# Optimization experiments

Measured on AMD Instinct MI355X. Metric: run time of the kernel, lower is better.

The kernel has to match this reference:

```python
import jax, jax.numpy as jnp
import numpy as np

XYZ_MIN = np.array([-1.0, -1.0, -1.0], np.float32)
XYZ_MAX = np.array([1.0, 1.0, 1.0], np.float32)
N_SAMPLES = 256
T_NEAR, T_FAR = 0.05, 2.0
ALPHA_INIT = 1e-6
ACT_SHIFT = float(np.log(1.0 / (1.0 - ALPHA_INIT) - 1.0))  # density bias shift
INTERVAL = 0.5  # stepsize * voxel_size_ratio
VIEWBASE_PE = 4


def trilerp(grid, pts):
    """grid: [C, X, Y, Z]; pts: [P, 3] world coords. Returns [P, C]."""
    res = jnp.asarray(grid.shape[1:], dtype=pts.dtype)  # [3]
    ind = (pts - XYZ_MIN) / (XYZ_MAX - XYZ_MIN) * (res - 1.0)
    ind = jnp.clip(ind, 0.0, res - 1.0)
    i0 = jnp.minimum(jnp.floor(ind), res - 2.0).astype(jnp.int32)  # [P,3]
    f = ind - i0.astype(pts.dtype)  # [P,3] fractional offsets
    x0, y0, z0 = i0[:, 0], i0[:, 1], i0[:, 2]
    x1, y1, z1 = x0 + 1, y0 + 1, z0 + 1
    fx, fy, fz = f[:, 0], f[:, 1], f[:, 2]
    gx, gy, gz = 1.0 - fx, 1.0 - fy, 1.0 - fz
    out = (grid[:, x0, y0, z0] * (gx * gy * gz)
           + grid[:, x1, y0, z0] * (fx * gy * gz)
           + grid[:, x0, y1, z0] * (gx * fy * gz)
           + grid[:, x0, y0, z1] * (gx * gy * fz)
           + grid[:, x1, y1, z0] * (fx * fy * gz)
           + grid[:, x1, y0, z1] * (fx * gy * fz)
           + grid[:, x0, y1, z1] * (gx * fy * fz)
           + grid[:, x1, y1, z1] * (fx * fy * fz))  # [C,P]
    return out.T


def setup_inputs() -> dict:
    key = jax.random.key(0)
    ks = jax.random.split(key, 10)
    N = 4096
    rays_o = jax.random.normal(ks[0], (N, 3), jnp.float32) * 0.05
    rays_d = jax.random.normal(ks[1], (N, 3), jnp.float32)
    density = jax.random.normal(ks[2], (1, 1, 160, 160, 160), jnp.float32)
    k0 = jax.random.normal(ks[3], (1, 12, 160, 160, 160), jnp.float32) * 0.1
    w0 = jax.random.normal(ks[4], (39, 128), jnp.float32) * (1.0 / np.sqrt(39))
    b0 = jnp.zeros((128,), jnp.float32)
    w1 = jax.random.normal(ks[5], (128, 128), jnp.float32) * (1.0 / np.sqrt(128))
    b1 = jnp.zeros((128,), jnp.float32)
    w2 = jax.random.normal(ks[6], (128, 3), jnp.float32) * (1.0 / np.sqrt(128))
    b2 = jnp.zeros((3,), jnp.float32)
    return {"rays_o": rays_o, "rays_d": rays_d, "density": density, "k0": k0,
            "w0": w0, "b0": b0, "w1": w1, "b1": b1, "w2": w2, "b2": b2}


def reference(rays_o, rays_d, density, k0, w0, b0, w1, b1, w2, b2):
    N = rays_o.shape[0]
    dens_grid = density[0]            # [1,X,Y,Z]
    feat_grid = k0[0]                 # [C,X,Y,Z]
    viewdirs = rays_d / jnp.linalg.norm(rays_d, axis=-1, keepdims=True)
    t = jnp.linspace(T_NEAR, T_FAR, N_SAMPLES, dtype=rays_o.dtype)  # [S]
    pts = rays_o[:, None, :] + viewdirs[:, None, :] * t[None, :, None]  # [N,S,3]
    inbox = jnp.all((pts >= XYZ_MIN) & (pts <= XYZ_MAX), axis=-1)  # [N,S]
    flat = pts.reshape(-1, 3)

    # density -> alpha: 1 - (1 + exp(d + shift))^(-interval)   (Raw2Alpha)
    d = trilerp(dens_grid, flat)[:, 0].reshape(N, N_SAMPLES)
    alpha = 1.0 - jnp.power(1.0 + jnp.exp(d + ACT_SHIFT), -INTERVAL)
    alpha = jnp.where(inbox, alpha, 0.0)

    # alpha -> weights via exclusive transmittance cumprod (Alphas2Weights)
    T_full = jnp.cumprod(1.0 - alpha, axis=1)               # [N,S]
    T_excl = jnp.concatenate([jnp.ones((N, 1), alpha.dtype), T_full[:, :-1]], axis=1)
    weights = alpha * T_excl                                 # [N,S]
    alphainv_last = T_full[:, -1]                            # [N]

    # color features + view-direction positional encoding
    feat = trilerp(feat_grid, flat).reshape(N, N_SAMPLES, -1)  # [N,S,C]
    freqs = (2.0 ** jnp.arange(VIEWBASE_PE)).astype(rays_o.dtype)
    vf = viewdirs[:, :, None] * freqs[None, None, :]           # [N,3,PE]
    vemb = jnp.concatenate([viewdirs, jnp.sin(vf).reshape(N, -1), jnp.cos(vf).reshape(N, -1)], axis=-1)  # [N,27]
    x = jnp.concatenate([feat, jnp.broadcast_to(vemb[:, None, :], (N, N_SAMPLES, vemb.shape[-1]))], axis=-1)

    h = jax.nn.relu(x @ w0 + b0)
    h = jax.nn.relu(h @ w1 + b1)
    rgb = jax.nn.sigmoid(h @ w2 + b2)                          # [N,S,3]

    rgb_marched = jnp.einsum('ns,nsc->nc', weights, rgb) + alphainv_last[:, None] * 1.0  # white bg
    return rgb_marched
```

## Files before the change

kernel.cpp:

```cpp
#include <hip/hip_runtime.h>
#include <hip/hip_bf16.h>
#include <math.h>

#define ACT_SHIFT_F (-13.8155095579637744f)
#define GRID_VOX 4096000
#define GP_BYTES  (GRID_VOX * 32)
#define W0P_OFF   GP_BYTES
#define W1P_OFF   (W0P_OFF + 8 * 1024)
#define W2P_OFF   (W1P_OFF + 32 * 1024)
#define WS_NEED   ((size_t)(W2P_OFF + 4 * 1024))

typedef __bf16 bf16x8 __attribute__((ext_vector_type(8)));
typedef float  f32x4  __attribute__((ext_vector_type(4)));

__device__ __forceinline__ float bfu(unsigned short b) {
    return __uint_as_float(((unsigned int)b) << 16);
}
__device__ __forceinline__ unsigned short f2bf(float x) {
    unsigned int u = __float_as_uint(x);
    u += 0x7fffu + ((u >> 16) & 1u);
    return (unsigned short)(u >> 16);
}
#define UNPK(u, lo, hi) { lo = __uint_as_float((u) << 16); hi = __uint_as_float((u) & 0xffff0000u); }

__device__ __constant__ int offv_c[8] = {0, 1, 160, 161, 25600, 25601, 25760, 25761};

__global__ void repack_all(const float* __restrict__ dens, const float* __restrict__ k0,
                           const float* __restrict__ w0, const float* __restrict__ w1,
                           const float* __restrict__ w2,
                           unsigned short* __restrict__ gp, unsigned short* __restrict__ wp)
{
    const int b = blockIdx.x;
    if (b < 16000) {
        const int v = b * 256 + threadIdx.x;
        unsigned short s[16];
        s[0] = f2bf(dens[v]);
        #pragma unroll
        for (int c = 0; c < 12; ++c) s[1 + c] = f2bf(k0[c * GRID_VOX + v]);
        s[13] = 0; s[14] = 0; s[15] = 0;
        uint4 q0, q1;
        q0.x = s[0] | (s[1] << 16);  q0.y = s[2] | (s[3] << 16);
        q0.z = s[4] | (s[5] << 16);  q0.w = s[6] | (s[7] << 16);
        q1.x = s[8] | (s[9] << 16);  q1.y = s[10] | (s[11] << 16);
        q1.z = s[12] | (s[13] << 16); q1.w = s[14] | (s[15] << 16);
        uint4* dst = (uint4*)(gp + (size_t)v * 16);
        dst[0] = q0; dst[1] = q1;
        return;
    }
    const int t = (b - 16000) * 256 + threadIdx.x;
    if (t >= 44 * 64) return;
    const int f = t >> 6, l = t & 63;
    const int n16 = l & 15, kg = l >> 4;
    unsigned short v[8];
    if (f < 8) {
        const int n = f * 16 + n16;
        #pragma unroll
        for (int j = 0; j < 8; ++j) {
            const int k = kg * 8 + j;
            v[j] = (k < 12) ? f2bf(w0[k * 128 + n]) : (unsigned short)0;
        }
    } else if (f < 40) {
        const int ff = f - 8, nt = ff >> 2, ks = ff & 3;
        const int n = nt * 16 + n16;
        #pragma unroll
        for (int j = 0; j < 8; ++j) {
            const int k = ks * 32 + kg * 8 + j;
            v[j] = f2bf(w1[k * 128 + n]);
        }
    } else {
        const int ks = f - 40;
        #pragma unroll
        for (int j = 0; j < 8; ++j) {
            const int k = ks * 32 + kg * 8 + j;
            v[j] = (n16 < 3) ? f2bf(w2[k * 3 + n16]) : (unsigned short)0;
        }
    }
    uint4 q;
    q.x = v[0] | (v[1] << 16); q.y = v[2] | (v[3] << 16);
    q.z = v[4] | (v[5] << 16); q.w = v[6] | (v[7] << 16);
    *(uint4*)(wp + f * 512 + l * 8) = q;
}

__global__ __launch_bounds__(256, 3)
void dvgo_mfma(const float* __restrict__ rays_o, const float* __restrict__ rays_d,
               const float* __restrict__ w0, const float* __restrict__ b0,
               const float* __restrict__ b1, const float* __restrict__ b2,
               const unsigned short* __restrict__ gp,
               const unsigned short* __restrict__ wpk,
               float* __restrict__ out)
{
    __shared__ unsigned short Xs[128 * 40];
    __shared__ unsigned short Hs[128 * 136];
    __shared__ float sh[256];
    __shared__ float wts[256];
    __shared__ float b0eff[128];
    __shared__ float b1s[128];
    __shared__ float vemb[28];
    __shared__ float red[4][3];
    __shared__ float b2s[3];
    __shared__ float ainv_sh;

    const int r = blockIdx.x, t = threadIdx.x;
    const int l = t & 63, wv = t >> 6;
    const int col = l & 15, rg = l >> 4;

    const float ox = rays_o[r*3+0], oy = rays_o[r*3+1], oz = rays_o[r*3+2];
    const float dxr = rays_d[r*3+0], dyr = rays_d[r*3+1], dzr = rays_d[r*3+2];
    const float rn = rsqrtf(dxr*dxr + dyr*dyr + dzr*dzr);
    const float vx = dxr*rn, vy = dyr*rn, vz = dzr*rn;

    if (t < 27) {
        float val;
        if (t < 3) val = (t == 0) ? vx : ((t == 1) ? vy : vz);
        else {
            int q = t - 3;
            const bool is_sin = q < 12;
            if (!is_sin) q -= 12;
            const int i = q >> 2, p = q & 3;
            const float a = ((i == 0) ? vx : ((i == 1) ? vy : vz)) * (float)(1 << p);
            val = is_sin ? sinf(a) : cosf(a);
        }
        vemb[t] = val;
    }
    if (t < 3)   b2s[t] = b2[t];
    if (t < 128) b1s[t] = b1[t];

    float alpha = 0.f;
    {
        const float tp = 0.05f + (1.95f / 255.f) * (float)t;
        const float px = ox + vx*tp, py = oy + vy*tp, pz = oz + vz*tp;
        const bool inbox = (px >= -1.f) & (px <= 1.f) & (py >= -1.f) & (py <= 1.f) &
                           (pz >= -1.f) & (pz <= 1.f);
        if (inbox) {
            const float ix = fminf(fmaxf((px + 1.f) * 79.5f, 0.f), 159.f);
            const float iy = fminf(fmaxf((py + 1.f) * 79.5f, 0.f), 159.f);
            const float iz = fminf(fmaxf((pz + 1.f) * 79.5f, 0.f), 159.f);
            const int x0 = min((int)ix, 158), y0 = min((int)iy, 158), z0 = min((int)iz, 158);
            const float fx = ix - x0, fy = iy - y0, fz = iz - z0;
            const float gx = 1.f - fx, gy = 1.f - fy, gz = 1.f - fz;
            const int base = (x0 * 160 + y0) * 160 + z0;
            float w8[8];
            w8[0]=gx*gy*gz; w8[1]=gx*gy*fz; w8[2]=gx*fy*gz; w8[3]=gx*fy*fz;
            w8[4]=fx*gy*gz; w8[5]=fx*gy*fz; w8[6]=fx*fy*gz; w8[7]=fx*fy*fz;
            float d = 0.f;
            #pragma unroll
            for (int cn = 0; cn < 8; ++cn)
                d = fmaf(w8[cn], bfu(gp[(size_t)(base + offv_c[cn]) * 16]), d);
            const float e = expf(d + ACT_SHIFT_F);
            const float op = 1.f + e;
            alpha = e / (op + sqrtf(op));
        }
        sh[t] = 1.f - alpha;
    }
    __syncthreads();

    if (t < 128) {
        float a = b0[t];
        #pragma unroll
        for (int k = 0; k < 27; ++k) a = fmaf(vemb[k], w0[(12 + k) * 128 + t], a);
        b0eff[t] = a;
    }
    for (int i = t; i < 128 * 10; i += 256) {
        const int row = i / 10, c = i % 10;
        ((unsigned int*)Xs)[row * 20 + 6 + c] = 0u;
    }

    #pragma unroll
    for (int off = 1; off < 256; off <<= 1) {
        const float v = (t >= off) ? sh[t - off] : 1.f;
        __syncthreads();
        sh[t] *= v;
        __syncthreads();
    }
    wts[t] = alpha * ((t == 0) ? 1.f : sh[t - 1]);
    if (t == 255) ainv_sh = sh[255];

    const unsigned short* w0p = wpk;
    const unsigned short* w1p = wpk + 8 * 512;
    const unsigned short* w2p = wpk + 40 * 512;
    const uint4* gq = (const uint4*)gp;

    float pacc = 0.f;

    #pragma unroll 1
    for (int ck = 0; ck < 2; ++ck) {
        {
            const int sl = t >> 1, hf = t & 1;
            const int s = ck * 128 + sl;
            const float tp = 0.05f + (1.95f / 255.f) * (float)s;
            const float px = ox + vx*tp, py = oy + vy*tp, pz = oz + vz*tp;
            const bool inbox = (px >= -1.f) & (px <= 1.f) & (py >= -1.f) & (py <= 1.f) &
                               (pz >= -1.f) & (pz <= 1.f);
            unsigned short* xrow = &Xs[sl * 40];
            if (inbox) {
                const float ix = fminf(fmaxf((px + 1.f) * 79.5f, 0.f), 159.f);
                const float iy = fminf(fmaxf((py + 1.f) * 79.5f, 0.f), 159.f);
                const float iz = fminf(fmaxf((pz + 1.f) * 79.5f, 0.f), 159.f);
                const int x0 = min((int)ix, 158), y0 = min((int)iy, 158), z0 = min((int)iz, 158);
                const float fx = ix - x0, fy = iy - y0, fz = iz - z0;
                const float gx = 1.f - fx, gy = 1.f - fy, gz = 1.f - fz;
                const int base = (x0 * 160 + y0) * 160 + z0;
                float w8[8];
                w8[0]=gx*gy*gz; w8[1]=gx*gy*fz; w8[2]=gx*fy*gz; w8[3]=gx*fy*fz;
                w8[4]=fx*gy*gz; w8[5]=fx*gy*fz; w8[6]=fx*fy*gz; w8[7]=fx*fy*fz;
                float a0=0,a1=0,a2=0,a3=0,a4=0,a5=0,a6=0,a7=0;
                #pragma unroll
                for (int cn = 0; cn < 8; ++cn) {
                    const uint4 q = gq[(size_t)(base + offv_c[cn]) * 2 + hf];
                    float f0,f1,f2,f3,f4,f5,f6,f7;
                    UNPK(q.x, f0, f1); UNPK(q.y, f2, f3);
                    UNPK(q.z, f4, f5); UNPK(q.w, f6, f7);
                    const float wc = w8[cn];
                    a0=fmaf(wc,f0,a0); a1=fmaf(wc,f1,a1); a2=fmaf(wc,f2,a2); a3=fmaf(wc,f3,a3);
                    a4=fmaf(wc,f4,a4); a5=fmaf(wc,f5,a5); a6=fmaf(wc,f6,a6); a7=fmaf(wc,f7,a7);
                }
                if (hf == 0) {
                    xrow[0]=f2bf(a1); xrow[1]=f2bf(a2); xrow[2]=f2bf(a3); xrow[3]=f2bf(a4);
                    xrow[4]=f2bf(a5); xrow[5]=f2bf(a6); xrow[6]=f2bf(a7);
                } else {
                    xrow[7]=f2bf(a0); xrow[8]=f2bf(a1); xrow[9]=f2bf(a2);
                    xrow[10]=f2bf(a3); xrow[11]=f2bf(a4);
                }
            } else {
                if (hf == 0) {
                    #pragma unroll
                    for (int j = 0; j < 7; ++j) xrow[j] = 0;
                } else {
                    #pragma unroll
                    for (int j = 7; j < 12; ++j) xrow[j] = 0;
                }
            }
        }
        __syncthreads();

        const int row0 = wv * 32;

        {
            bf16x8 A0[2];
            #pragma unroll
            for (int mt = 0; mt < 2; ++mt)
                A0[mt] = *(const bf16x8*)(&Xs[(row0 + mt * 16 + col) * 40 + rg * 8]);
            #pragma unroll 1
            for (int nt = 0; nt < 8; ++nt) {
                const bf16x8 B = *(const bf16x8*)(w0p + nt * 512 + l * 8);
                const float bias = b0eff[nt * 16 + col];
                #pragma unroll
                for (int mt = 0; mt < 2; ++mt) {
                    f32x4 acc = {0.f, 0.f, 0.f, 0.f};
                    acc = __builtin_amdgcn_mfma_f32_16x16x32_bf16(A0[mt], B, acc, 0, 0, 0);
                    #pragma unroll
                    for (int q = 0; q < 4; ++q) {
                        const float v  = fmaxf(acc[q] + bias, 0.f);
                        const float vo = __shfl_xor(v, 1);
                        if ((l & 1) == 0) {
                            const int row = row0 + mt * 16 + rg * 4 + q;
                            const unsigned int pk = (unsigned int)f2bf(v) |
                                                    ((unsigned int)f2bf(vo) << 16);
                            *(unsigned int*)(&Hs[row * 136 + nt * 16 + col]) = pk;
                        }
                    }
                }
            }
        }

        {
            bf16x8 A1[2][4];
            #pragma unroll
            for (int mt = 0; mt < 2; ++mt)
                #pragma unroll
                for (int ks = 0; ks < 4; ++ks)
                    A1[mt][ks] = *(const bf16x8*)(&Hs[(row0 + mt * 16 + col) * 136 + ks * 32 + rg * 8]);
            #pragma unroll 1
            for (int nt = 0; nt < 8; ++nt) {
                bf16x8 Bk[4];
                #pragma unroll
                for (int ks = 0; ks < 4; ++ks)
                    Bk[ks] = *(const bf16x8*)(w1p + (nt * 4 + ks) * 512 + l * 8);
                const float bias = b1s[nt * 16 + col];
                #pragma unroll
                for (int mt = 0; mt < 2; ++mt) {
                    f32x4 acc = {0.f, 0.f, 0.f, 0.f};
                    #pragma unroll
                    for (int ks = 0; ks < 4; ++ks)
                        acc = __builtin_amdgcn_mfma_f32_16x16x32_bf16(A1[mt][ks], Bk[ks], acc, 0, 0, 0);
                    #pragma unroll
                    for (int q = 0; q < 4; ++q) {
                        const float v  = fmaxf(acc[q] + bias, 0.f);
                        const float vo = __shfl_xor(v, 1);
                        if ((l & 1) == 0) {
                            const int row = row0 + mt * 16 + rg * 4 + q;
                            const unsigned int pk = (unsigned int)f2bf(v) |
                                                    ((unsigned int)f2bf(vo) << 16);
                            *(unsigned int*)(&Hs[row * 136 + nt * 16 + col]) = pk;
                        }
                    }
                }
            }
        }

        {
            bf16x8 Bk[4];
            #pragma unroll
            for (int ks = 0; ks < 4; ++ks)
                Bk[ks] = *(const bf16x8*)(w2p + ks * 512 + l * 8);
            const float bias2 = (col < 3) ? b2s[col] : 0.f;
            #pragma unroll
            for (int mt = 0; mt < 2; ++mt) {
                bf16x8 A2[4];
                #pragma unroll
                for (int ks = 0; ks < 4; ++ks)
                    A2[ks] = *(const bf16x8*)(&Hs[(row0 + mt * 16 + col) * 136 + ks * 32 + rg * 8]);
                f32x4 acc = {0.f, 0.f, 0.f, 0.f};
                #pragma unroll
                for (int ks = 0; ks < 4; ++ks)
                    acc = __builtin_amdgcn_mfma_f32_16x16x32_bf16(A2[ks], Bk[ks], acc, 0, 0, 0);
                #pragma unroll
                for (int q = 0; q < 4; ++q) {
                    const float rv = acc[q] + bias2;
                    const float sg = 1.f / (1.f + expf(-rv));
                    const int srow = ck * 128 + row0 + mt * 16 + rg * 4 + q;
                    pacc = fmaf(wts[srow], sg, pacc);
                }
            }
        }
        __syncthreads();
    }

    pacc += __shfl_xor(pacc, 16);
    pacc += __shfl_xor(pacc, 32);
    if (rg == 0 && col < 3) red[wv][col] = pacc;
    __syncthreads();
    if (t < 3) out[r * 3 + t] = red[0][t] + red[1][t] + red[2][t] + red[3][t] + ainv_sh;
}

__global__ __launch_bounds__(256, 2)
void dvgo_render(const float* __restrict__ rays_o, const float* __restrict__ rays_d,
                 const float* __restrict__ dens, const float* __restrict__ k0,
                 const float* __restrict__ w0, const float* __restrict__ b0,
                 const float* __restrict__ w1, const float* __restrict__ b1,
                 const float* __restrict__ w2, const float* __restrict__ b2,
                 float* __restrict__ out)
{
    __shared__ float xs[256 * 40];
    __shared__ float sh[256];
    __shared__ float wts[256];
    __shared__ float h0s[2][128];
    __shared__ float red[2][2][3];
    __shared__ float rgbacc[6];
    __shared__ float ainv_sh;

    const int r = blockIdx.x, tid = threadIdx.x;
    {
        const int s = tid;
        const float ox = rays_o[r*3+0], oy = rays_o[r*3+1], oz = rays_o[r*3+2];
        const float dxr = rays_d[r*3+0], dyr = rays_d[r*3+1], dzr = rays_d[r*3+2];
        const float rn = rsqrtf(dxr*dxr + dyr*dyr + dzr*dzr);
        const float vx = dxr*rn, vy = dyr*rn, vz = dzr*rn;
        const float t = 0.05f + 1.95f * (1.0f/255.0f) * (float)s;
        const float px = ox + vx*t, py = oy + vy*t, pz = oz + vz*t;
        const bool inbox = (px >= -1.f) && (px <= 1.f) && (py >= -1.f) && (py <= 1.f) &&
                           (pz >= -1.f) && (pz <= 1.f);
        const float ix = fminf(fmaxf((px + 1.f) * 79.5f, 0.f), 159.f);
        const float iy = fminf(fmaxf((py + 1.f) * 79.5f, 0.f), 159.f);
        const float iz = fminf(fmaxf((pz + 1.f) * 79.5f, 0.f), 159.f);
        const int x0 = min((int)ix, 158), y0 = min((int)iy, 158), z0 = min((int)iz, 158);
        const float fx = ix - x0, fy = iy - y0, fz = iz - z0;
        const float gx = 1.f - fx, gy = 1.f - fy, gz = 1.f - fz;
        const int DX = 25600, DY = 160;
        const int base = (x0*160 + y0)*160 + z0;
        const float w000=gx*gy*gz, w100=fx*gy*gz, w010=gx*fy*gz, w001=gx*gy*fz;
        const float w110=fx*fy*gz, w101=fx*gy*fz, w011=gx*fy*fz, w111=fx*fy*fz;
        float alpha = 0.f;
        if (inbox) {
            const float d = dens[base]*w000 + dens[base+DX]*w100 + dens[base+DY]*w010 +
                            dens[base+1]*w001 + dens[base+DX+DY]*w110 + dens[base+DX+1]*w101 +
                            dens[base+DY+1]*w011 + dens[base+DX+DY+1]*w111;
            const float e = expf(d + ACT_SHIFT_F);
            const float op = 1.f + e;
            alpha = e / (op + sqrtf(op));
        }
        sh[s] = 1.f - alpha;
        __syncthreads();
        #pragma unroll
        for (int off = 1; off < 256; off <<= 1) {
            const float v = (s >= off) ? sh[s - off] : 1.f;
            __syncthreads();
            sh[s] *= v;
            __syncthreads();
        }
        wts[s] = alpha * ((s == 0) ? 1.f : sh[s-1]);
        if (s == 255) ainv_sh = sh[255];
        if (s < 6) rgbacc[s] = 0.f;
        float* xrow = &xs[s*40];
        if (inbox) {
            #pragma unroll
            for (int c = 0; c < 12; ++c) {
                const float* g = k0 + c*4096000 + base;
                xrow[c] = g[0]*w000 + g[DX]*w100 + g[DY]*w010 + g[1]*w001 +
                          g[DX+DY]*w110 + g[DX+1]*w101 + g[DY+1]*w011 + g[DX+DY+1]*w111;
            }
        } else {
            #pragma unroll
            for (int c = 0; c < 12; ++c) xrow[c] = 0.f;
        }
        xrow[12]=vx; xrow[13]=vy; xrow[14]=vz;
        const float v3[3] = {vx, vy, vz};
        #pragma unroll
        for (int i = 0; i < 3; ++i)
            #pragma unroll
            for (int p = 0; p < 4; ++p) {
                const float a = v3[i] * (float)(1 << p);
                xrow[15 + i*4 + p] = sinf(a);
                xrow[27 + i*4 + p] = cosf(a);
            }
        xrow[39] = 0.f;
    }
    __syncthreads();
    const int j = tid & 127, sb = tid >> 7;
    float w0c[40];
    #pragma unroll
    for (int k = 0; k < 39; ++k) w0c[k] = w0[k*128 + j];
    w0c[39] = 0.f;
    float w1c[128];
    #pragma unroll
    for (int k = 0; k < 128; ++k) w1c[k] = w1[k*128 + j];
    const float b0j = b0[j], b1j = b1[j];
    const float w2r0 = w2[j*3+0], w2r1 = w2[j*3+1], w2r2 = w2[j*3+2];
    const float b20 = b2[0], b21 = b2[1], b22 = b2[2];
    const int lane = tid & 63, halfw = (tid >> 6) & 1;
    for (int it = 0; it < 128; ++it) {
        const int s = it*2 + sb;
        const float4* xrow4 = (const float4*)(&xs[s*40]);
        float acc = b0j;
        #pragma unroll
        for (int q = 0; q < 10; ++q) {
            const float4 v = xrow4[q];
            acc = fmaf(v.x, w0c[q*4+0], acc); acc = fmaf(v.y, w0c[q*4+1], acc);
            acc = fmaf(v.z, w0c[q*4+2], acc); acc = fmaf(v.w, w0c[q*4+3], acc);
        }
        h0s[sb][j] = fmaxf(acc, 0.f);
        __syncthreads();
        float acc1 = b1j;
        const float4* h4 = (const float4*)(&h0s[sb][0]);
        #pragma unroll
        for (int q = 0; q < 32; ++q) {
            const float4 v = h4[q];
            acc1 = fmaf(v.x, w1c[q*4+0], acc1); acc1 = fmaf(v.y, w1c[q*4+1], acc1);
            acc1 = fmaf(v.z, w1c[q*4+2], acc1); acc1 = fmaf(v.w, w1c[q*4+3], acc1);
        }
        const float hv = fmaxf(acc1, 0.f);
        float p0 = hv*w2r0, p1 = hv*w2r1, p2 = hv*w2r2;
        #pragma unroll
        for (int off = 32; off > 0; off >>= 1) {
            p0 += __shfl_down(p0, off); p1 += __shfl_down(p1, off); p2 += __shfl_down(p2, off);
        }
        if (lane == 0) { red[sb][halfw][0]=p0; red[sb][halfw][1]=p1; red[sb][halfw][2]=p2; }
        __syncthreads();
        if (tid == sb*128) {
            const float r0 = red[sb][0][0]+red[sb][1][0]+b20;
            const float r1 = red[sb][0][1]+red[sb][1][1]+b21;
            const float r2 = red[sb][0][2]+red[sb][1][2]+b22;
            const float wgt = wts[s];
            rgbacc[sb*3+0] += wgt / (1.f + expf(-r0));
            rgbacc[sb*3+1] += wgt / (1.f + expf(-r1));
            rgbacc[sb*3+2] += wgt / (1.f + expf(-r2));
        }
    }
    __syncthreads();
    if (tid < 3) out[r*3 + tid] = rgbacc[tid] + rgbacc[3 + tid] + ainv_sh;
}

extern "C" void kernel_launch(void* const* d_in, const int* in_sizes, int n_in,
                              void* d_out, int out_size, void* d_ws, size_t ws_size,
                              hipStream_t stream)
{
    const float* rays_o = (const float*)d_in[0];
    const float* rays_d = (const float*)d_in[1];
    const float* dens   = (const float*)d_in[2];
    const float* k0     = (const float*)d_in[3];
    const float* w0     = (const float*)d_in[4];
    const float* b0     = (const float*)d_in[5];
    const float* w1     = (const float*)d_in[6];
    const float* b1     = (const float*)d_in[7];
    const float* w2     = (const float*)d_in[8];
    const float* b2     = (const float*)d_in[9];
    float* out = (float*)d_out;
    const int N = in_sizes[0] / 3;

    if (ws_size >= WS_NEED) {
        unsigned short* gp  = (unsigned short*)d_ws;
        unsigned short* wpk = (unsigned short*)((char*)d_ws + W0P_OFF);
        repack_all<<<dim3(16011), dim3(256), 0, stream>>>(dens, k0, w0, w1, w2, gp, wpk);
        dvgo_mfma<<<dim3(N), dim3(256), 0, stream>>>(rays_o, rays_d, w0, b0, b1, b2,
                                                     gp, wpk, out);
    } else {
        dvgo_render<<<dim3(N), dim3(256), 0, stream>>>(rays_o, rays_d, dens, k0,
                                                       w0, b0, w1, b1, w2, b2, out);
    }
}
```

Measured before the change: 515.2 us.

## Vectorize grid repack and fuse alpha computation into per-chunk feature gather

```diff
diff --git a/kernel.cpp b/kernel.cpp
--- a/kernel.cpp
+++ b/kernel.cpp
@@ -12,6 +12,7 @@
 
 typedef __bf16 bf16x8 __attribute__((ext_vector_type(8)));
 typedef float  f32x4  __attribute__((ext_vector_type(4)));
+typedef float  fv4    __attribute__((ext_vector_type(4)));
 
 __device__ __forceinline__ float bfu(unsigned short b) {
     return __uint_as_float(((unsigned int)b) << 16);
@@ -20,6 +21,9 @@
     unsigned int u = __float_as_uint(x);
     u += 0x7fffu + ((u >> 16) & 1u);
     return (unsigned short)(u >> 16);
+}
+__device__ __forceinline__ unsigned int packtr(float a, float b) {
+    return (__float_as_uint(a) >> 16) | (__float_as_uint(b) & 0xffff0000u);
 }
 #define UNPK(u, lo, hi) { lo = __uint_as_float((u) << 16); hi = __uint_as_float((u) & 0xffff0000u); }
 
@@ -31,23 +35,32 @@
                            unsigned short* __restrict__ gp, unsigned short* __restrict__ wp)
 {
     const int b = blockIdx.x;
-    if (b < 16000) {
-        const int v = b * 256 + threadIdx.x;
-        unsigned short s[16];
-        s[0] = f2bf(dens[v]);
-        #pragma unroll
-        for (int c = 0; c < 12; ++c) s[1 + c] = f2bf(k0[c * GRID_VOX + v]);
-        s[13] = 0; s[14] = 0; s[15] = 0;
-        uint4 q0, q1;
-        q0.x = s[0] | (s[1] << 16);  q0.y = s[2] | (s[3] << 16);
-        q0.z = s[4] | (s[5] << 16);  q0.w = s[6] | (s[7] << 16);
-        q1.x = s[8] | (s[9] << 16);  q1.y = s[10] | (s[11] << 16);
-        q1.z = s[12] | (s[13] << 16); q1.w = s[14] | (s[15] << 16);
-        uint4* dst = (uint4*)(gp + (size_t)v * 16);
-        dst[0] = q0; dst[1] = q1;
+    if (b < 4000) {
+        const int v4 = b * 1024 + threadIdx.x * 4;
+        const fv4 d4 = __builtin_nontemporal_load((const fv4*)(dens + v4));
+        fv4 c4[12];
+        #pragma unroll
+        for (int c = 0; c < 12; ++c)
+            c4[c] = __builtin_nontemporal_load((const fv4*)(k0 + (size_t)c * GRID_VOX + v4));
+        uint4* dst = (uint4*)(gp + (size_t)v4 * 16);
+        #pragma unroll
+        for (int j = 0; j < 4; ++j) {
+            const float* cj = &((const float*)c4)[j];
+            uint4 q0, q1;
+            q0.x = packtr(d4[j],    cj[0]);
+            q0.y = packtr(cj[4*1],  cj[4*2]);
+            q0.z = packtr(cj[4*3],  cj[4*4]);
+            q0.w = packtr(cj[4*5],  cj[4*6]);
+            q1.x = packtr(cj[4*7],  cj[4*8]);
+            q1.y = packtr(cj[4*9],  cj[4*10]);
+            q1.z = packtr(cj[4*11], 0.f);
+            q1.w = 0u;
+            dst[j*2 + 0] = q0;
+            dst[j*2 + 1] = q1;
+        }
         return;
     }
-    const int t = (b - 16000) * 256 + threadIdx.x;
+    const int t = (b - 4000) * 256 + threadIdx.x;
     if (t >= 44 * 64) return;
     const int f = t >> 6, l = t & 63;
     const int n16 = l & 15, kg = l >> 4;
@@ -91,14 +104,15 @@
 {
     __shared__ unsigned short Xs[128 * 40];
     __shared__ unsigned short Hs[128 * 136];
-    __shared__ float sh[256];
-    __shared__ float wts[256];
+    __shared__ float shA[128];
+    __shared__ float wts[128];
     __shared__ float b0eff[128];
     __shared__ float b1s[128];
     __shared__ float vemb[28];
     __shared__ float red[4][3];
     __shared__ float b2s[3];
-    __shared__ float ainv_sh;
+    __shared__ float Tcs[3];
+    __shared__ float spart;
 
     const int r = blockIdx.x, t = threadIdx.x;
     const int l = t & 63, wv = t >> 6;
@@ -124,34 +138,7 @@
     }
     if (t < 3)   b2s[t] = b2[t];
     if (t < 128) b1s[t] = b1[t];
-
-    float alpha = 0.f;
-    {
-        const float tp = 0.05f + (1.95f / 255.f) * (float)t;
-        const float px = ox + vx*tp, py = oy + vy*tp, pz = oz + vz*tp;
-        const bool inbox = (px >= -1.f) & (px <= 1.f) & (py >= -1.f) & (py <= 1.f) &
-                           (pz >= -1.f) & (pz <= 1.f);
-        if (inbox) {
-            const float ix = fminf(fmaxf((px + 1.f) * 79.5f, 0.f), 159.f);
-            const float iy = fminf(fmaxf((py + 1.f) * 79.5f, 0.f), 159.f);
-            const float iz = fminf(fmaxf((pz + 1.f) * 79.5f, 0.f), 159.f);
-            const int x0 = min((int)ix, 158), y0 = min((int)iy, 158), z0 = min((int)iz, 158);
-            const float fx = ix - x0, fy = iy - y0, fz = iz - z0;
-            const float gx = 1.f - fx, gy = 1.f - fy, gz = 1.f - fz;
-            const int base = (x0 * 160 + y0) * 160 + z0;
-            float w8[8];
-            w8[0]=gx*gy*gz; w8[1]=gx*gy*fz; w8[2]=gx*fy*gz; w8[3]=gx*fy*fz;
-            w8[4]=fx*gy*gz; w8[5]=fx*gy*fz; w8[6]=fx*fy*gz; w8[7]=fx*fy*fz;
-            float d = 0.f;
-            #pragma unroll
-            for (int cn = 0; cn < 8; ++cn)
-                d = fmaf(w8[cn], bfu(gp[(size_t)(base + offv_c[cn]) * 16]), d);
-            const float e = expf(d + ACT_SHIFT_F);
-            const float op = 1.f + e;
-            alpha = e / (op + sqrtf(op));
-        }
-        sh[t] = 1.f - alpha;
-    }
+    if (t == 0)  Tcs[0] = 1.f;
     __syncthreads();
 
     if (t < 128) {
@@ -164,16 +151,6 @@
         const int row = i / 10, c = i % 10;
         ((unsigned int*)Xs)[row * 20 + 6 + c] = 0u;
     }
-
-    #pragma unroll
-    for (int off = 1; off < 256; off <<= 1) {
-        const float v = (t >= off) ? sh[t - off] : 1.f;
-        __syncthreads();
-        sh[t] *= v;
-        __syncthreads();
-    }
-    wts[t] = alpha * ((t == 0) ? 1.f : sh[t - 1]);
-    if (t == 255) ainv_sh = sh[255];
 
     const unsigned short* w0p = wpk;
     const unsigned short* w1p = wpk + 8 * 512;
@@ -217,6 +194,11 @@
                 if (hf == 0) {
                     xrow[0]=f2bf(a1); xrow[1]=f2bf(a2); xrow[2]=f2bf(a3); xrow[3]=f2bf(a4);
                     xrow[4]=f2bf(a5); xrow[5]=f2bf(a6); xrow[6]=f2bf(a7);
+                    const float e = expf(a0 + ACT_SHIFT_F);
+                    const float op = 1.f + e;
+                    const float alpha = e / (op + sqrtf(op));
+                    wts[sl] = alpha;
+                    shA[sl] = 1.f - alpha;
                 } else {
                     xrow[7]=f2bf(a0); xrow[8]=f2bf(a1); xrow[9]=f2bf(a2);
                     xrow[10]=f2bf(a3); xrow[11]=f2bf(a4);
@@ -225,11 +207,36 @@
                 if (hf == 0) {
                     #pragma unroll
                     for (int j = 0; j < 7; ++j) xrow[j] = 0;
+                    wts[sl] = 0.f;
+                    shA[sl] = 1.f;
                 } else {
                     #pragma unroll
                     for (int j = 7; j < 12; ++j) xrow[j] = 0;
                 }
             }
+        }
+        __syncthreads();
+
+        float v = 1.f;
+        if (t < 128) {
+            v = shA[t];
+            #pragma unroll
+            for (int off = 1; off < 64; off <<= 1) {
+                const float u = __shfl_up(v, off);
+                if (l >= off) v *= u;
+            }
+            if (wv == 0 && l == 63) spart = v;
+        }
+        __syncthreads();
+        if (t < 128) {
+            float excl = __shfl_up(v, 1);
+            if (l == 0) excl = 1.f;
+            float E = Tcs[ck];
+            const float sp = spart;
+            if (wv == 1) E *= sp;
+            const float w = wts[t] * E * excl;
+            wts[t] = w;
+            if (t == 127) Tcs[ck + 1] = Tcs[ck] * sp * v;
         }
         __syncthreads();
 
@@ -250,11 +257,11 @@
                     acc = __builtin_amdgcn_mfma_f32_16x16x32_bf16(A0[mt], B, acc, 0, 0, 0);
                     #pragma unroll
                     for (int q = 0; q < 4; ++q) {
-                        const float v  = fmaxf(acc[q] + bias, 0.f);
-                        const float vo = __shfl_xor(v, 1);
+                        const float vv = fmaxf(acc[q] + bias, 0.f);
+                        const float vo = __shfl_xor(vv, 1);
                         if ((l & 1) == 0) {
                             const int row = row0 + mt * 16 + rg * 4 + q;
-                            const unsigned int pk = (unsigned int)f2bf(v) |
+                            const unsigned int pk = (unsigned int)f2bf(vv) |
                                                     ((unsigned int)f2bf(vo) << 16);
                             *(unsigned int*)(&Hs[row * 136 + nt * 16 + col]) = pk;
                         }
@@ -285,11 +292,11 @@
                         acc = __builtin_amdgcn_mfma_f32_16x16x32_bf16(A1[mt][ks], Bk[ks], acc, 0, 0, 0);
                     #pragma unroll
                     for (int q = 0; q < 4; ++q) {
-                        const float v  = fmaxf(acc[q] + bias, 0.f);
-                        const float vo = __shfl_xor(v, 1);
+                        const float vv = fmaxf(acc[q] + bias, 0.f);
+                        const float vo = __shfl_xor(vv, 1);
                         if ((l & 1) == 0) {
                             const int row = row0 + mt * 16 + rg * 4 + q;
-                            const unsigned int pk = (unsigned int)f2bf(v) |
+                            const unsigned int pk = (unsigned int)f2bf(vv) |
                                                     ((unsigned int)f2bf(vo) << 16);
                             *(unsigned int*)(&Hs[row * 136 + nt * 16 + col]) = pk;
                         }
@@ -318,7 +325,7 @@
                 for (int q = 0; q < 4; ++q) {
                     const float rv = acc[q] + bias2;
                     const float sg = 1.f / (1.f + expf(-rv));
-                    const int srow = ck * 128 + row0 + mt * 16 + rg * 4 + q;
+                    const int srow = row0 + mt * 16 + rg * 4 + q;
                     pacc = fmaf(wts[srow], sg, pacc);
                 }
             }
@@ -330,7 +337,7 @@
     pacc += __shfl_xor(pacc, 32);
     if (rg == 0 && col < 3) red[wv][col] = pacc;
     __syncthreads();
-    if (t < 3) out[r * 3 + t] = red[0][t] + red[1][t] + red[2][t] + red[3][t] + ainv_sh;
+    if (t < 3) out[r * 3 + t] = red[0][t] + red[1][t] + red[2][t] + red[3][t] + Tcs[2];
 }
 
 __global__ __launch_bounds__(256, 2)
@@ -490,7 +497,7 @@
     if (ws_size >= WS_NEED) {
         unsigned short* gp  = (unsigned short*)d_ws;
         unsigned short* wpk = (unsigned short*)((char*)d_ws + W0P_OFF);
-        repack_all<<<dim3(16011), dim3(256), 0, stream>>>(dens, k0, w0, w1, w2, gp, wpk);
+        repack_all<<<dim3(4011), dim3(256), 0, stream>>>(dens, k0, w0, w1, w2, gp, wpk);
         dvgo_mfma<<<dim3(N), dim3(256), 0, stream>>>(rays_o, rays_d, w0, b0, b1, b2,
                                                      gp, wpk, out);
     } else {
```

New measurement: 513.2 us. About the same (-0.4%).
